# Performance work log

Measured on AMD Instinct MI355X. Metric: run time of the kernel, lower is better.

## Reference

```python
import jax, jax.numpy as jnp
import numpy as np

B, C, T_LEN, T_LAT = 32, 512, 1024, 31
T = T_LAT + 1          # t_len_block
NB = T_LEN // T        # n_blocks (t_pad == 0 by construction)
FS_SCALE = 10.0        # FastSigmoid surrogate scale

@jax.custom_vjp
def spike_fs(x):
    return (x > 0).astype(x.dtype)

def _fs_fwd(x):
    return (x > 0).astype(x.dtype), x

def _fs_bwd(x, g):
    return (g / (FS_SCALE * jnp.abs(x) + 1.0) ** 2,)

spike_fs.defvjp(_fs_fwd, _fs_bwd)

def _g(z):
    # keep entries exactly == 1, zero others; gradient passes through identically
    return z - jax.lax.stop_gradient(jnp.where(z == 1.0, 0.0, z))

def setup_inputs() -> dict:
    key = jax.random.key(0)
    k1, k2, k3, k4, k5 = jax.random.split(key, 5)
    x = jax.random.normal(k1, (B, C, T_LEN), jnp.float32)
    beta_raw = jax.random.uniform(k2, (C,), jnp.float32, 0.8, 0.95)   # _beta param
    rec_weight = jnp.eye(C, dtype=jnp.float32) + 0.05 * jax.random.normal(k3, (C, C), jnp.float32)
    p_raw = jax.random.uniform(k4, (C,), jnp.float32, 0.7, 0.95)      # _p param
    b_raw = jax.random.uniform(k5, (C,), jnp.float32, 0.3, 0.7)       # _b param
    return {"x": x, "beta_raw": beta_raw, "rec_weight": rec_weight, "p_raw": p_raw, "b_raw": b_raw}

def _forward(x, beta_raw, rec_weight, p_raw, b_raw):
    dt = x.dtype
    beta = jnp.clip(beta_raw, 0.001, 0.999)
    p = jnp.clip(jnp.abs(p_raw), 0.0, 0.999)
    b = jnp.clip(jnp.abs(b_raw), 0.001, 1.0)

    idx = jnp.arange(T)
    tril = idx[:, None] >= idx[None, :]
    # causal decay kernel: K[c,t,s] = beta_c**(t-s) for s<=t (== bconv1d with beta kernel)
    K = jnp.where(tril[None], beta[:, None, None] ** jnp.maximum(idx[:, None] - idx[None, :], 0).astype(dt), 0.0)
    # phi kernel: z[t] = sum_{s<=t} spikes[s] * (t-s+1)
    Zm = jnp.where(tril, (idx[:, None] - idx[None, :] + 1).astype(dt), 0.0)
    p_pow = p[:, None] ** jnp.arange(1, T + 1, dtype=dt)[None, :]  # (C,T)

    def block(cur, v_init, v_th):
        cur = cur.at[:, :, 0].add(beta[None, :] * v_init)
        mem = jnp.einsum('cts,bcs->bct', K, cur)          # (B,C,T)
        fs = spike_fs(mem - v_th)
        z = jnp.einsum('ts,bcs->bct', Zm, fs)
        return _g(z), z, mem

    Bx = x.shape[0]
    x_blocks = x.reshape(Bx, C, NB, T).transpose(2, 0, 1, 3)  # (NB,B,C,T)

    spikes0, z0, mem0 = block(x_blocks[0], jnp.zeros((Bx, C), dt), jnp.ones((Bx, C, T), dt))
    a_kernel0 = jnp.zeros((Bx, C, T), dt)

    def body(carry, x_slice):
        spikes_prev, z_prev, mem_last, a_kernel = carry
        sp_det = jax.lax.stop_gradient(spikes_prev)          # detach_spike_grad=True
        x_slice = x_slice + jnp.einsum('ij,bjt->bit', rec_weight, sp_det)
        mask_f = (jnp.max(sp_det, axis=2) != 0.0).astype(dt)  # (B,C) spike mask
        x_slice = jnp.where(z_prev < mask_f[:, :, None], 0.0, x_slice)  # refractory suppression
        v_init = mem_last * (1.0 - mask_f)
        # adaptation
        a_at_spike = jnp.sum(a_kernel * sp_det, axis=2) + 1.0 / p[None, :]
        decay_steps = jnp.sum((z_prev > 1.0).astype(dt), axis=2)
        new_a = a_at_spike * p[None, :] ** decay_steps
        a = a_kernel[:, :, -1] * (1.0 - mask_f) + new_a * mask_f
        a_kernel = p_pow[None] * a[:, :, None]               # (B,C,T)
        v_th = 1.0 + b[None, :, None] * a_kernel
        spikes, z, mem = block(x_slice, v_init, v_th)
        return (spikes, z, mem[:, :, -1], a_kernel), spikes

    carry0 = (spikes0, z0, mem0[:, :, -1], a_kernel0)
    _, spikes_rest = jax.lax.scan(body, carry0, x_blocks[1:])
    all_spikes = jnp.concatenate([spikes0[None], spikes_rest], axis=0)  # (NB,B,C,T)
    return all_spikes.transpose(1, 2, 0, 3).reshape(Bx, C, NB * T)

def reference(x, beta_raw, rec_weight, p_raw, b_raw):
    return _forward(x, beta_raw, rec_weight, p_raw, b_raw)
```

## Files before the change

kernel.cpp:

```cpp
#include <hip/hip_runtime.h>
#include <stdint.h>
#include <stddef.h>

#define CH     512
#define TT     32
#define NBLK   32
#define NBATCH 32
#define NCHUNK 8
#define NTHR   1024

__global__ __launch_bounds__(256) void transpose_k(const float* __restrict__ W,
                                                   float* __restrict__ WT) {
    __shared__ float tile[64][65];
    const int bx = blockIdx.x & 7, by = blockIdx.x >> 3;
    const int lx = threadIdx.x & 63, ly = threadIdx.x >> 6;
    for (int r = ly; r < 64; r += 4)
        tile[r][lx] = W[(size_t)(by * 64 + r) * CH + bx * 64 + lx];
    __syncthreads();
    for (int r = ly; r < 64; r += 4)
        WT[(size_t)(bx * 64 + r) * CH + by * 64 + lx] = tile[lx][r];
}

__global__ __launch_bounds__(NTHR, 4) void snn_kernel(
    const float* __restrict__ x,
    const float* __restrict__ beta_raw,
    const float* __restrict__ WT,
    const float* __restrict__ p_raw,
    const float* __restrict__ b_raw,
    int*       __restrict__ ent_g,
    float*     __restrict__ out)
{
    __shared__ float rec8[8][2112];
    __shared__ float rec_tot[2112];
    __shared__ int   tf_lds[64];
    __shared__ int   tmp16[64];

    const int bidx = blockIdx.x;
    const int b    = bidx & (NBATCH - 1);
    const int kown = bidx >> 5;
    const int tid  = threadIdx.x;
    const int l    = tid & 63;
    const int g    = tid >> 6;
    const size_t base = ((size_t)b) << 19;
    int* pg = ent_g + (b << 9);

    const int c = (kown << 6) + l;
    const float beta  = fminf(fmaxf(beta_raw[c], 0.001f), 0.999f);
    const float p     = fminf(fabsf(p_raw[c]), 0.999f);
    const float bb    = fminf(fmaxf(fabsf(b_raw[c]), 0.001f), 1.0f);
    const float inv_p = 1.0f / p;
    float p32; { float t2 = p*p, t4 = t2*t2, t8 = t4*t4, t16 = t8*t8; p32 = t16*t16; }
    float a_mult = 0.f, v_init = 0.f;
    int   zero_start = 0;
    const unsigned long long lowmask = (1ull << l) - 1ull;

    if (tid < 512) {
        const int ch = tid >> 3, q = tid & 7;
        const float4 v = *(const float4*)(x + base + ((size_t)((kown << 6) + ch) << 10) + (q << 2));
        float* d = &rec8[0][ch * 33 + (q << 2)];
        d[0] = v.x; d[1] = v.y; d[2] = v.z; d[3] = v.w;
    } else {
        const int t0 = tid - 512;
        #pragma unroll
        for (int z = 0; z < 29; ++z) {
            const int k = t0 + (z << 9);
            if (k < 14784) (&rec8[1][0])[k] = 0.f;
        }
    }
    __syncthreads();

    for (int n = 0; n < NBLK; ++n) {
        float4 xstage;
        if (g >= 8) {
            const int slot = tid - 512;
            const int ch = slot >> 3, q = slot & 7;
            if (n + 1 < NBLK)
                xstage = *(const float4*)(x + base + ((size_t)((kown << 6) + ch) << 10) + ((n + 1) << 5) + (q << 2));
            if (n > 0) {
                const int tf = tf_lds[ch];
                const int t0 = q << 2;
                float4 v;
                v.x = (t0     == tf) ? 1.f : 0.f;
                v.y = (t0 + 1 == tf) ? 1.f : 0.f;
                v.z = (t0 + 2 == tf) ? 1.f : 0.f;
                v.w = (t0 + 3 == tf) ? 1.f : 0.f;
                *(float4*)(out + base + ((size_t)((kown << 6) + ch) << 10) + ((n - 1) << 5) + t0) = v;
            }
        } else if (n > 0) {
            const int* pgr = pg + (((n - 1) & 1) << 8);
            const unsigned want = (unsigned)((n - 1) & 15);
            const int l31 = l & 31;
            const char* WTb = (const char*)WT;
            const int col4 = ((kown << 6) + l) << 2;
            float* myrec = &rec8[g][l * 33];
            int pf = 0;
            float acc = 0.f; int cur_t = -1;
            #pragma unroll 1
            for (int j = 0; j < 8; ++j) {
                int wv;
                while (true) {
                    wv = __hip_atomic_load(pgr + (j << 5) + l31,
                                           __ATOMIC_RELAXED, __HIP_MEMORY_SCOPE_AGENT);
                    const unsigned v = (unsigned)wv;
                    const bool ok = ((((v >> 12) & 15u) == want) && (((v >> 28) & 15u) == want));
                    if (__all(ok)) break;
                    __builtin_amdgcn_s_sleep(1);
                }
                const int elo = wv & 0xFFFF, ehi = (wv >> 16) & 0xFFFF;
                const unsigned long long blo = __ballot((l < 32) && (((elo >> 6) & 63) != 63));
                const unsigned long long bhi = __ballot((l < 32) && (((ehi >> 6) & 63) != 63));
                const int cnt = (int)__popcll(blo) + (int)__popcll(bhi);
                const int off   = (g - pf) & 7;
                const int mycnt = (cnt > off) ? ((cnt - off + 7) >> 3) : 0;
                int T[8]; float F[8];
                #pragma unroll
                for (int k = 0; k < 8; ++k) {
                    const int r  = off + (k << 3);
                    const bool ok2 = k < mycnt;
                    const int w  = __builtin_amdgcn_readlane(wv, r >> 1);
                    const int e  = (r & 1) ? ((w >> 16) & 0xFFFF) : (w & 0xFFFF);
                    T[k] = ok2 ? ((e >> 6) & 31) : -1;
                    const int ch = ok2 ? ((j << 6) | (e & 63)) : 0;
                    F[k] = *(const float*)(WTb + (ch << 11) + col4);
                }
                #pragma unroll
                for (int k = 0; k < 8; ++k) {
                    if (T[k] >= 0) {
                        if (T[k] != cur_t) { if (cur_t >= 0) myrec[cur_t] += acc; acc = 0.f; cur_t = T[k]; }
                        acc += F[k];
                    }
                }
                pf += cnt;
            }
            if (cur_t >= 0) myrec[cur_t] += acc;
        }
        __syncthreads();

        #pragma unroll
        for (int r = 0; r < 2; ++r) {
            const int e = tid + (r << 10);
            const int idx = ((e >> 5) * 33) + (e & 31);
            rec_tot[idx] = ((rec8[0][idx] + rec8[1][idx]) + (rec8[2][idx] + rec8[3][idx]))
                         + ((rec8[4][idx] + rec8[5][idx]) + (rec8[6][idx] + rec8[7][idx]));
        }
        __syncthreads();

        if (g == 0) {
            __builtin_amdgcn_s_setprio(1);
            float mem = 0.f, pc = p, pca = p;
            int t_first = -1, mypos = 0;
            unsigned prefc = 0;
            #pragma unroll
            for (int t = 0; t < TT; ++t) {
                const float rv = rec_tot[l * 33 + t];
                float cur = (t >= zero_start) ? rv : 0.f;
                if (t == 0) cur += beta * v_init;
                mem = beta * mem + cur;
                const float vth = 1.f + bb * pc * a_mult;
                const bool fire = (mem - vth > 0.f) && (t_first < 0);
                const unsigned long long bal = __ballot(fire);
                if (fire) {
                    t_first = t; pca = pc;
                    mypos = (int)prefc + (int)__popcll(bal & lowmask);
                }
                prefc += (unsigned)__popcll(bal);
                pc *= p;
            }
            if (t_first >= 0) {
                float pd = 1.f;
                for (int m = 31 - t_first; m > 0; --m) pd *= p;
                a_mult = (pca * a_mult + inv_p) * pd;
                v_init = 0.f; zero_start = t_first;
            } else {
                a_mult = p32 * a_mult;
                v_init = mem; zero_start = 0;
            }
            tf_lds[l] = t_first;
            if (n + 1 < NBLK) {
                const bool sp = (t_first >= 0);
                const unsigned long long balS = __ballot(sp);
                const int cntS = (int)prefc;
                if (!sp) mypos = cntS + (int)__popcll(~balS & lowmask);
                const int tval = sp ? t_first : 63;
                tmp16[mypos] = ((n & 15) << 12) | (tval << 6) | l;
                __threadfence_block();
                if (l < 32) {
                    const int wlo = tmp16[l << 1];
                    const int whi = tmp16[(l << 1) | 1];
                    __hip_atomic_store(pg + ((n & 1) << 8) + (kown << 5) + l, wlo | (whi << 16),
                                       __ATOMIC_RELAXED, __HIP_MEMORY_SCOPE_AGENT);
                }
            }
            __builtin_amdgcn_s_setprio(0);
        } else if (g >= 8) {
            if (n + 1 < NBLK) {
                const int slot = tid - 512;
                const int ch = slot >> 3, q = slot & 7;
                float* d = &rec8[0][ch * 33 + (q << 2)];
                d[0] = xstage.x; d[1] = xstage.y; d[2] = xstage.z; d[3] = xstage.w;
            }
        } else {
            if (n + 1 < NBLK) {
                const int t0 = tid - 64;
                #pragma unroll
                for (int z = 0; z < 33; ++z)
                    (&rec8[1][0])[t0 + 448 * z] = 0.f;
            }
        }
        __syncthreads();
    }

    if (tid < 512) {
        const int ch = tid >> 3, q = tid & 7;
        const int tf = tf_lds[ch];
        const int t0 = q << 2;
        float4 v;
        v.x = (t0     == tf) ? 1.f : 0.f;
        v.y = (t0 + 1 == tf) ? 1.f : 0.f;
        v.z = (t0 + 2 == tf) ? 1.f : 0.f;
        v.w = (t0 + 3 == tf) ? 1.f : 0.f;
        *(float4*)(out + base + ((size_t)((kown << 6) + ch) << 10) + (31 << 5) + t0) = v;
    }
}

extern "C" void kernel_launch(void* const* d_in, const int* in_sizes, int n_in,
                              void* d_out, int out_size, void* d_ws, size_t ws_size,
                              hipStream_t stream) {
    (void)in_sizes; (void)n_in; (void)out_size;
    const float* x   = (const float*)d_in[0];
    const float* br  = (const float*)d_in[1];
    const float* W   = (const float*)d_in[2];
    const float* pr  = (const float*)d_in[3];
    const float* bbr = (const float*)d_in[4];
    float* out = (float*)d_out;

    const size_t wt_bytes  = (size_t)CH * CH * sizeof(float);
    const size_t ent_bytes = (size_t)NBATCH * 512 * sizeof(int);
    if (ws_size < wt_bytes + ent_bytes) return;

    float* WT    = (float*)d_ws;
    int*   ent_g = (int*)((char*)d_ws + wt_bytes);

    transpose_k<<<64, 256, 0, stream>>>(W, WT);
    snn_kernel<<<NBATCH * NCHUNK, NTHR, 0, stream>>>(x, br, WT, pr, bbr, ent_g, out);
}
```

Measured before the change: 578.4 us.

## Process each batch in one workgroup, removing cross-block spin-wait exchange

Replaces the 8-workgroups-per-batch split, which exchanged spike entries through global memory with atomic spin-waits, with a single 1024-thread workgroup per batch that holds all 512 channels in double-buffered LDS. Spike lists are compacted in LDS, and each channel thread accumulates recurrent weights directly into its own row, so the 8-way partial reduction and extra barrier go away. The cost is only 32 workgroups on the device, eight of 16 waves doing the serial recurrence, and a larger LDS footprint per workgroup.

```diff
diff --git a/kernel.cpp b/kernel.cpp
--- a/kernel.cpp
+++ b/kernel.cpp
@@ -6,7 +6,6 @@
 #define TT     32
 #define NBLK   32
 #define NBATCH 32
-#define NCHUNK 8
 #define NTHR   1024
 
 __global__ __launch_bounds__(256) void transpose_k(const float* __restrict__ W,
@@ -27,143 +26,114 @@
     const float* __restrict__ WT,
     const float* __restrict__ p_raw,
     const float* __restrict__ b_raw,
-    int*       __restrict__ ent_g,
     float*     __restrict__ out)
 {
-    __shared__ float rec8[8][2112];
-    __shared__ float rec_tot[2112];
-    __shared__ int   tf_lds[64];
-    __shared__ int   tmp16[64];
-
-    const int bidx = blockIdx.x;
-    const int b    = bidx & (NBATCH - 1);
-    const int kown = bidx >> 5;
-    const int tid  = threadIdx.x;
-    const int l    = tid & 63;
-    const int g    = tid >> 6;
+    __shared__ float buf[2][CH * 33];
+    __shared__ __align__(16) int ent[512];
+    __shared__ int cnt_lds[8];
+    __shared__ int tf2[2][CH];
+
+    const int b   = blockIdx.x;
+    const int tid = threadIdx.x;
+    const int l   = tid & 63;
+    const int g   = tid >> 6;
     const size_t base = ((size_t)b) << 19;
-    int* pg = ent_g + (b << 9);
-
-    const int c = (kown << 6) + l;
-    const float beta  = fminf(fmaxf(beta_raw[c], 0.001f), 0.999f);
-    const float p     = fminf(fabsf(p_raw[c]), 0.999f);
-    const float bb    = fminf(fmaxf(fabsf(b_raw[c]), 0.001f), 1.0f);
+
+    const int c  = (g << 6) + l;
+    const int cc = c & (CH - 1);
+    const float beta  = fminf(fmaxf(beta_raw[cc], 0.001f), 0.999f);
+    const float p     = fminf(fabsf(p_raw[cc]), 0.999f);
+    const float bb    = fminf(fmaxf(fabsf(b_raw[cc]), 0.001f), 1.0f);
     const float inv_p = 1.0f / p;
     float p32; { float t2 = p*p, t4 = t2*t2, t8 = t4*t4, t16 = t8*t8; p32 = t16*t16; }
     float a_mult = 0.f, v_init = 0.f;
     int   zero_start = 0;
     const unsigned long long lowmask = (1ull << l) - 1ull;
 
-    if (tid < 512) {
-        const int ch = tid >> 3, q = tid & 7;
-        const float4 v = *(const float4*)(x + base + ((size_t)((kown << 6) + ch) << 10) + (q << 2));
-        float* d = &rec8[0][ch * 33 + (q << 2)];
-        d[0] = v.x; d[1] = v.y; d[2] = v.z; d[3] = v.w;
-    } else {
-        const int t0 = tid - 512;
+    if (g >= 8) {
+        const int slot = tid - 512, q = slot & 7, ch0 = slot >> 3;
         #pragma unroll
-        for (int z = 0; z < 29; ++z) {
-            const int k = t0 + (z << 9);
-            if (k < 14784) (&rec8[1][0])[k] = 0.f;
+        for (int it = 0; it < 8; ++it) {
+            const int ch = ch0 + (it << 6);
+            const float4 v = *(const float4*)(x + base + ((size_t)ch << 10) + (q << 2));
+            float* d = &buf[0][ch * 33 + (q << 2)];
+            d[0] = v.x; d[1] = v.y; d[2] = v.z; d[3] = v.w;
         }
     }
     __syncthreads();
 
+    #pragma unroll 1
     for (int n = 0; n < NBLK; ++n) {
-        float4 xstage;
+        float* bufc = &buf[n & 1][0];
+        float4 xs[8];
+
         if (g >= 8) {
-            const int slot = tid - 512;
-            const int ch = slot >> 3, q = slot & 7;
-            if (n + 1 < NBLK)
-                xstage = *(const float4*)(x + base + ((size_t)((kown << 6) + ch) << 10) + ((n + 1) << 5) + (q << 2));
+            const int slot = tid - 512, q = slot & 7, ch0 = slot >> 3;
             if (n > 0) {
-                const int tf = tf_lds[ch];
-                const int t0 = q << 2;
-                float4 v;
-                v.x = (t0     == tf) ? 1.f : 0.f;
-                v.y = (t0 + 1 == tf) ? 1.f : 0.f;
-                v.z = (t0 + 2 == tf) ? 1.f : 0.f;
-                v.w = (t0 + 3 == tf) ? 1.f : 0.f;
-                *(float4*)(out + base + ((size_t)((kown << 6) + ch) << 10) + ((n - 1) << 5) + t0) = v;
+                #pragma unroll
+                for (int it = 0; it < 8; ++it) {
+                    const int ch = ch0 + (it << 6);
+                    const int tf = tf2[(n - 1) & 1][ch];
+                    const int t0 = q << 2;
+                    float4 v;
+                    v.x = (t0     == tf) ? 1.f : 0.f;
+                    v.y = (t0 + 1 == tf) ? 1.f : 0.f;
+                    v.z = (t0 + 2 == tf) ? 1.f : 0.f;
+                    v.w = (t0 + 3 == tf) ? 1.f : 0.f;
+                    *(float4*)(out + base + ((size_t)ch << 10) + ((n - 1) << 5) + t0) = v;
+                }
+            }
+            if (n + 1 < NBLK) {
+                #pragma unroll
+                for (int it = 0; it < 8; ++it) {
+                    const int ch = ch0 + (it << 6);
+                    xs[it] = *(const float4*)(x + base + ((size_t)ch << 10) + ((n + 1) << 5) + (q << 2));
+                }
             }
         } else if (n > 0) {
-            const int* pgr = pg + (((n - 1) & 1) << 8);
-            const unsigned want = (unsigned)((n - 1) & 15);
-            const int l31 = l & 31;
             const char* WTb = (const char*)WT;
-            const int col4 = ((kown << 6) + l) << 2;
-            float* myrec = &rec8[g][l * 33];
-            int pf = 0;
+            const int col4 = c << 2;
+            float* myrec = &bufc[c * 33];
             float acc = 0.f; int cur_t = -1;
             #pragma unroll 1
             for (int j = 0; j < 8; ++j) {
-                int wv;
-                while (true) {
-                    wv = __hip_atomic_load(pgr + (j << 5) + l31,
-                                           __ATOMIC_RELAXED, __HIP_MEMORY_SCOPE_AGENT);
-                    const unsigned v = (unsigned)wv;
-                    const bool ok = ((((v >> 12) & 15u) == want) && (((v >> 28) & 15u) == want));
-                    if (__all(ok)) break;
-                    __builtin_amdgcn_s_sleep(1);
-                }
-                const int elo = wv & 0xFFFF, ehi = (wv >> 16) & 0xFFFF;
-                const unsigned long long blo = __ballot((l < 32) && (((elo >> 6) & 63) != 63));
-                const unsigned long long bhi = __ballot((l < 32) && (((ehi >> 6) & 63) != 63));
-                const int cnt = (int)__popcll(blo) + (int)__popcll(bhi);
-                const int off   = (g - pf) & 7;
-                const int mycnt = (cnt > off) ? ((cnt - off + 7) >> 3) : 0;
-                int T[8]; float F[8];
-                #pragma unroll
-                for (int k = 0; k < 8; ++k) {
-                    const int r  = off + (k << 3);
-                    const bool ok2 = k < mycnt;
-                    const int w  = __builtin_amdgcn_readlane(wv, r >> 1);
-                    const int e  = (r & 1) ? ((w >> 16) & 0xFFFF) : (w & 0xFFFF);
-                    T[k] = ok2 ? ((e >> 6) & 31) : -1;
-                    const int ch = ok2 ? ((j << 6) | (e & 63)) : 0;
-                    F[k] = *(const float*)(WTb + (ch << 11) + col4);
-                }
-                #pragma unroll
-                for (int k = 0; k < 8; ++k) {
-                    if (T[k] >= 0) {
-                        if (T[k] != cur_t) { if (cur_t >= 0) myrec[cur_t] += acc; acc = 0.f; cur_t = T[k]; }
-                        acc += F[k];
+                const int cj = cnt_lds[j];
+                const int Ew = ent[(j << 6) + l];
+                for (int r0 = 0; r0 < cj; r0 += 16) {
+                    int T[16]; float F[16];
+                    #pragma unroll
+                    for (int k = 0; k < 16; ++k) {
+                        const int r = r0 + k;
+                        const int e = __builtin_amdgcn_readlane(Ew, r & 63);
+                        const bool ok = r < cj;
+                        T[k] = ok ? (e & 31) : -1;
+                        const int off = ok ? ((e & ~31) << 6) : 0;
+                        F[k] = *(const float*)(WTb + off + col4);
                     }
-                }
-                pf += cnt;
+                    #pragma unroll
+                    for (int k = 0; k < 16; ++k) {
+                        if (T[k] >= 0) {
+                            if (T[k] != cur_t) { if (cur_t >= 0) myrec[cur_t] += acc; acc = 0.f; cur_t = T[k]; }
+                            acc += F[k];
+                        }
+                    }
+                }
             }
             if (cur_t >= 0) myrec[cur_t] += acc;
         }
         __syncthreads();
 
-        #pragma unroll
-        for (int r = 0; r < 2; ++r) {
-            const int e = tid + (r << 10);
-            const int idx = ((e >> 5) * 33) + (e & 31);
-            rec_tot[idx] = ((rec8[0][idx] + rec8[1][idx]) + (rec8[2][idx] + rec8[3][idx]))
-                         + ((rec8[4][idx] + rec8[5][idx]) + (rec8[6][idx] + rec8[7][idx]));
-        }
-        __syncthreads();
-
-        if (g == 0) {
-            __builtin_amdgcn_s_setprio(1);
+        if (g < 8) {
             float mem = 0.f, pc = p, pca = p;
-            int t_first = -1, mypos = 0;
-            unsigned prefc = 0;
+            int t_first = -1;
             #pragma unroll
             for (int t = 0; t < TT; ++t) {
-                const float rv = rec_tot[l * 33 + t];
+                const float rv = bufc[c * 33 + t];
                 float cur = (t >= zero_start) ? rv : 0.f;
                 if (t == 0) cur += beta * v_init;
                 mem = beta * mem + cur;
                 const float vth = 1.f + bb * pc * a_mult;
-                const bool fire = (mem - vth > 0.f) && (t_first < 0);
-                const unsigned long long bal = __ballot(fire);
-                if (fire) {
-                    t_first = t; pca = pc;
-                    mypos = (int)prefc + (int)__popcll(bal & lowmask);
-                }
-                prefc += (unsigned)__popcll(bal);
+                if ((mem - vth > 0.f) && t_first < 0) { t_first = t; pca = pc; }
                 pc *= p;
             }
             if (t_first >= 0) {
@@ -175,51 +145,45 @@
                 a_mult = p32 * a_mult;
                 v_init = mem; zero_start = 0;
             }
-            tf_lds[l] = t_first;
-            if (n + 1 < NBLK) {
-                const bool sp = (t_first >= 0);
-                const unsigned long long balS = __ballot(sp);
-                const int cntS = (int)prefc;
-                if (!sp) mypos = cntS + (int)__popcll(~balS & lowmask);
-                const int tval = sp ? t_first : 63;
-                tmp16[mypos] = ((n & 15) << 12) | (tval << 6) | l;
-                __threadfence_block();
-                if (l < 32) {
-                    const int wlo = tmp16[l << 1];
-                    const int whi = tmp16[(l << 1) | 1];
-                    __hip_atomic_store(pg + ((n & 1) << 8) + (kown << 5) + l, wlo | (whi << 16),
-                                       __ATOMIC_RELAXED, __HIP_MEMORY_SCOPE_AGENT);
-                }
-            }
-            __builtin_amdgcn_s_setprio(0);
-        } else if (g >= 8) {
-            if (n + 1 < NBLK) {
-                const int slot = tid - 512;
-                const int ch = slot >> 3, q = slot & 7;
-                float* d = &rec8[0][ch * 33 + (q << 2)];
-                d[0] = xstage.x; d[1] = xstage.y; d[2] = xstage.z; d[3] = xstage.w;
-            }
+            tf2[n & 1][c] = t_first;
+            unsigned prefc = 0; int mypos = 0;
+            #pragma unroll
+            for (int t = 0; t < TT; ++t) {
+                const unsigned long long bal = __ballot(t_first == t);
+                if (t_first == t) mypos = (int)prefc + (int)__popcll(bal & lowmask);
+                prefc += (unsigned)__popcll(bal);
+            }
+            if (t_first >= 0) ent[(g << 6) + mypos] = (c << 5) | t_first;
+            if (l == 0) cnt_lds[g] = (int)prefc;
         } else {
             if (n + 1 < NBLK) {
-                const int t0 = tid - 64;
+                const int slot = tid - 512, q = slot & 7, ch0 = slot >> 3;
+                float* bufn = &buf[(n + 1) & 1][0];
                 #pragma unroll
-                for (int z = 0; z < 33; ++z)
-                    (&rec8[1][0])[t0 + 448 * z] = 0.f;
+                for (int it = 0; it < 8; ++it) {
+                    const int ch = ch0 + (it << 6);
+                    float* d = &bufn[ch * 33 + (q << 2)];
+                    d[0] = xs[it].x; d[1] = xs[it].y; d[2] = xs[it].z; d[3] = xs[it].w;
+                }
             }
         }
         __syncthreads();
     }
 
-    if (tid < 512) {
-        const int ch = tid >> 3, q = tid & 7;
-        const int tf = tf_lds[ch];
-        const int t0 = q << 2;
-        float4 v;
-        v.x = (t0     == tf) ? 1.f : 0.f;
-        v.y = (t0 + 1 == tf) ? 1.f : 0.f;
-        v.z = (t0 + 2 == tf) ? 1.f : 0.f;
-        v.w = (t0 + 3 == tf) ? 1.f : 0.f;
-        *(float4*)(out + base + ((size_t)((kown << 6) + ch) << 10) + (31 << 5) + t0) = v;
+    {
+        const int q = tid & 7, ch0 = tid >> 3;
+        #pragma unroll
+        for (int it = 0; it < 4; ++it) {
+            const int ch = ch0 + (it << 7);
+            const int tf = tf2[1][ch];
+            const int t0 = q << 2;
+            float4 v;
+            v.x = (t0     == tf) ? 1.f : 0.f;
+            v.y = (t0 + 1 == tf) ? 1.f : 0.f;
+            v.z = (t0 + 2 == tf) ? 1.f : 0.f;
+            v.w = (t0 + 3 == tf) ? 1.f : 0.f;
+            *(float4*)(out + base + ((size_t)ch << 10) + (31 << 5) + t0) = v;
+        }
     }
 }
 
@@ -234,13 +198,10 @@
     const float* bbr = (const float*)d_in[4];
     float* out = (float*)d_out;
 
-    const size_t wt_bytes  = (size_t)CH * CH * sizeof(float);
-    const size_t ent_bytes = (size_t)NBATCH * 512 * sizeof(int);
-    if (ws_size < wt_bytes + ent_bytes) return;
-
-    float* WT    = (float*)d_ws;
-    int*   ent_g = (int*)((char*)d_ws + wt_bytes);
+    const size_t wt_bytes = (size_t)CH * CH * sizeof(float);
+    if (ws_size < wt_bytes) return;
+    float* WT = (float*)d_ws;
 
     transpose_k<<<64, 256, 0, stream>>>(W, WT);
-    snn_kernel<<<NBATCH * NCHUNK, NTHR, 0, stream>>>(x, br, WT, pr, bbr, ent_g, out);
+    snn_kernel<<<NBATCH, NTHR, 0, stream>>>(x, br, WT, pr, bbr, out);
 }
```

After: 1.541 ms. +166.4%, slower.
